# Performance work log

Measured on AMD Instinct MI355X. Metric: run time of the kernel, lower is better.

Reference implementation:

```python
import jax, jax.numpy as jnp
import numpy as np

N, NFEAT, NHID, NHEADS, NCLASS = 4096, 64, 64, 4, 64
ALPHA = 0.2        # LeakyReLU negative slope
NEG = -9.0e15      # mask value from the torch code (-9e15)


def _xavier(key, shape, gain=1.414):
    fan_in, fan_out = shape[-2] if len(shape) > 1 else shape[-1], shape[-1]
    if len(shape) == 1:
        fan_in, fan_out = shape[0], 1
    bound = gain * np.sqrt(6.0 / (fan_in + fan_out))
    return jax.random.uniform(key, shape, jnp.float32, -bound, bound)


def setup_inputs() -> dict:
    key = jax.random.key(0)
    ks = jax.random.split(key, 6)
    x = jax.random.normal(ks[0], (N, NFEAT), jnp.float32)
    # sparse-ish adjacency mask with self loops (adj > 0 gating in torch code)
    adj = jax.random.bernoulli(ks[1], 0.02, (N, N)) | jnp.eye(N, dtype=bool)
    W_heads = _xavier(ks[2], (NHEADS, NFEAT, NHID))                  # per-head W
    a_heads = _xavier(ks[3], (NHEADS, 2 * NHID))                     # per-head a (flattened [2F',1])
    W_out = _xavier(ks[4], (NHEADS * NHID, NCLASS))
    a_out = _xavier(ks[5], (2 * NCLASS,))
    return {"x": x, "W_heads": W_heads, "a_heads": a_heads,
            "W_out": W_out, "a_out": a_out, "adj": adj}


def gat_layer(x, adj, W, a, concat):
    # h: [N, F']
    h = x @ W
    Fp = h.shape[-1]
    # e_ij = leakyrelu(a[:F'].h_i + a[F':].h_j)  == torch's cat([h_i, h_j]) @ a
    f1 = h @ a[:Fp]                 # [N]
    f2 = h @ a[Fp:]                 # [N]
    e = jax.nn.leaky_relu(f1[:, None] + f2[None, :], ALPHA)   # [N, N]
    att = jax.nn.softmax(jnp.where(adj, e, NEG), axis=1)      # row softmax over neighbors
    hp = att @ h                    # [N, F']
    return jax.nn.elu(hp) if concat else hp


def reference(x, W_heads, a_heads, W_out, a_out, adj):
    # multi-head GAT with concat (dropout omitted: eval mode)
    heads = jax.vmap(lambda W, a: gat_layer(x, adj, W, a, True))(W_heads, a_heads)  # [H, N, F']
    hcat = jnp.transpose(heads, (1, 0, 2)).reshape(x.shape[0], NHEADS * NHID)       # [N, H*F']
    out = gat_layer(hcat, adj, W_out, a_out, False)                                  # [N, nclass]
    return out
```

## Files before the change

kernel.cpp:

```cpp
#include <hip/hip_runtime.h>
#include <hip/hip_fp16.h>

#define N 4096
#define CAP 160
#define ALPHA 0.2f
#define NSCAN 1024

__device__ __forceinline__ float wred_sum(float v) {
#pragma unroll
  for (int o = 32; o > 0; o >>= 1) v += __shfl_xor(v, o, 64);
  return v;
}

__device__ __forceinline__ void h8_fma(float4 raw, float p, float* acc) {
  union { float4 f4; __half2 h2[4]; } u;
  u.f4 = raw;
#pragma unroll
  for (int t = 0; t < 4; ++t) {
    float2 v = __half22float2(u.h2[t]);
    acc[2 * t]     = fmaf(p, v.x, acc[2 * t]);
    acc[2 * t + 1] = fmaf(p, v.y, acc[2 * t + 1]);
  }
}

__global__ void stage1_k(const void* __restrict__ adjv, const float* __restrict__ x,
                         const float* __restrict__ W, const float* __restrict__ a,
                         int* __restrict__ cnt, int* __restrict__ cols,
                         __half* __restrict__ h1, float* __restrict__ f1h,
                         float* __restrict__ f2h) {
  __shared__ float Ws[64 * 64];
  __shared__ float xs[4][64];
  int bid = blockIdx.x;
  int tid = threadIdx.x;
  int lane = tid & 63;
  if (bid < NSCAN) {
    int w = tid >> 6;
    int i = bid * 4 + w;
    int* mycols = cols + (size_t)i * CAP;
    const unsigned char* adjB = (const unsigned char*)adjv;
    bool byteLayout = (adjB[(size_t)N + 1] == 1);
    unsigned long long lt = (lane == 0) ? 0ull : (~0ull >> (64 - lane));
    int base = 0;
#define SCAN_ROUND(cond, jj)                                              \
    {                                                                     \
      unsigned long long m = __ballot(cond);                              \
      if (cond) {                                                         \
        int p = base + __popcll(m & lt);                                  \
        if (p < CAP) mycols[p] = (jj);                                    \
      }                                                                   \
      base += __popcll(m);                                                \
    }
    if (byteLayout) {
      const uint4* row4 = (const uint4*)(adjB + (size_t)i * N);
      uint4 v0 = row4[lane];
      uint4 v1 = row4[64 + lane];
      uint4 v2 = row4[128 + lane];
      uint4 v3 = row4[192 + lane];
#define SCAN_WORD(u, j0)                                                  \
      SCAN_ROUND(((u) & 0xffu) != 0, (j0));                               \
      SCAN_ROUND(((u) & 0xff00u) != 0, (j0) + 1);                         \
      SCAN_ROUND(((u) & 0xff0000u) != 0, (j0) + 2);                       \
      SCAN_ROUND(((u) & 0xff000000u) != 0, (j0) + 3);
#define SCAN_UINT4(v, it)                                                 \
      {                                                                   \
        int j0 = ((it) * 64 + lane) * 16;                                 \
        SCAN_WORD((v).x, j0);                                             \
        SCAN_WORD((v).y, j0 + 4);                                         \
        SCAN_WORD((v).z, j0 + 8);                                         \
        SCAN_WORD((v).w, j0 + 12);                                        \
      }
      SCAN_UINT4(v0, 0);
      SCAN_UINT4(v1, 1);
      SCAN_UINT4(v2, 2);
      SCAN_UINT4(v3, 3);
    } else {
      const int4* row = (const int4*)((const int*)adjv + (size_t)i * N);
      int4 nxt = row[lane];
      for (int it = 0; it < 16; ++it) {
        int4 cur = nxt;
        if (it < 15) nxt = row[(it + 1) * 64 + lane];
        int j0 = (it * 64 + lane) * 4;
        SCAN_ROUND(cur.x != 0, j0);
        SCAN_ROUND(cur.y != 0, j0 + 1);
        SCAN_ROUND(cur.z != 0, j0 + 2);
        SCAN_ROUND(cur.w != 0, j0 + 3);
      }
    }
    if (lane == 0) cnt[i] = min(base, CAP);
#undef SCAN_UINT4
#undef SCAN_WORD
#undef SCAN_ROUND
  } else {
    int u = bid - NSCAN;
    int h = u & 3;
    int r = tid >> 6, f = lane;
    int n = (u >> 2) * 4 + r;
    const float4* W4 = (const float4*)(W + h * 4096);
    float4* Ws4 = (float4*)Ws;
    for (int t = tid; t < 1024; t += 256) Ws4[t] = W4[t];
    xs[r][f] = x[(size_t)n * 64 + f];
    __syncthreads();
    float acc = 0.f;
#pragma unroll
    for (int k = 0; k < 64; k += 4) {
      float4 xk = *(const float4*)&xs[r][k];
      acc = fmaf(xk.x, Ws[k * 64 + f], acc);
      acc = fmaf(xk.y, Ws[(k + 1) * 64 + f], acc);
      acc = fmaf(xk.z, Ws[(k + 2) * 64 + f], acc);
      acc = fmaf(xk.w, Ws[(k + 3) * 64 + f], acc);
    }
    h1[((size_t)h * N + n) * 64 + f] = __float2half(acc);
    float s1 = wred_sum(acc * a[h * 128 + f]);
    float s2 = wred_sum(acc * a[h * 128 + 64 + f]);
    if (f == 0) { f1h[n * 4 + h] = s1; f2h[n * 4 + h] = s2; }
  }
}

__global__ void attn1_gemm_k(const int* __restrict__ cnt, const int* __restrict__ cols,
                             const __half* __restrict__ h1,
                             const float* __restrict__ f1g,
                             const float* __restrict__ f2g,
                             const float* __restrict__ Wout,
                             const float* __restrict__ aout,
                             __half* __restrict__ h2, float* __restrict__ f1o,
                             float* __restrict__ f2o) {
  int i0 = blockIdx.x * 2;
  int i1 = i0 + 1;
  int tid = threadIdx.x;
  int w = tid >> 6, lane = tid & 63;
  __shared__ int cS[2][CAP];
  __shared__ float pS[2][4][CAP];
  __shared__ float red[4][2][4];
  __shared__ float sDinv[2][4];
  __shared__ float hrow[2][256];
  __shared__ float4 part4[2][4][16];
  int c0 = cnt[i0], c1 = cnt[i1];
  float4 t10 = ((const float4*)f1g)[i0];
  float4 t11 = ((const float4*)f1g)[i1];
  float f1r[2][4] = {{t10.x, t10.y, t10.z, t10.w}, {t11.x, t11.y, t11.z, t11.w}};
  float dloc[2][4] = {{0.f, 0.f, 0.f, 0.f}, {0.f, 0.f, 0.f, 0.f}};
#pragma unroll
  for (int rr = 0; rr < 2; ++rr) {
    int c = rr ? c1 : c0;
    int ii = rr ? i1 : i0;
    for (int k = tid; k < c; k += 256) {
      int j = cols[(size_t)ii * CAP + k];
      cS[rr][k] = j;
      float4 t2 = ((const float4*)f2g)[j];
      float f2v[4] = {t2.x, t2.y, t2.z, t2.w};
#pragma unroll
      for (int h = 0; h < 4; ++h) {
        float s = f1r[rr][h] + f2v[h];
        s = s > 0.f ? s : ALPHA * s;
        float p = __expf(s);
        pS[rr][h][k] = p;
        dloc[rr][h] += p;
      }
    }
  }
#pragma unroll
  for (int rr = 0; rr < 2; ++rr)
#pragma unroll
    for (int h = 0; h < 4; ++h) {
      float d = wred_sum(dloc[rr][h]);
      if (lane == 0) red[w][rr][h] = d;
    }
  __syncthreads();
  if (tid < 8) {
    int rr = tid >> 2, h = tid & 3;
    float d = red[0][rr][h] + red[1][rr][h] + red[2][rr][h] + red[3][rr][h];
    int c = rr ? c1 : c0;
    sDinv[rr][h] = (c > 0) ? 1.f / d : 0.f;
  }
  __syncthreads();
  int g = lane >> 3, ff = lane & 7, h = w;
  const __half* hb = h1 + ((size_t)h * N) * 64;
  float a0[8] = {0.f, 0.f, 0.f, 0.f, 0.f, 0.f, 0.f, 0.f};
  float a1[8] = {0.f, 0.f, 0.f, 0.f, 0.f, 0.f, 0.f, 0.f};
  int cmax = c0 > c1 ? c0 : c1;
#pragma unroll 2
  for (int k0 = 0; k0 < cmax; k0 += 8) {
    int k = k0 + g;
    bool o0 = k < c0, o1 = k < c1;
    int j0 = o0 ? cS[0][k] : 0, j1 = o1 ? cS[1][k] : 0;
    float p0 = o0 ? pS[0][h][k] : 0.f, p1 = o1 ? pS[1][h][k] : 0.f;
    float4 r0 = *(const float4*)(hb + (size_t)j0 * 64 + ff * 8);
    float4 r1 = *(const float4*)(hb + (size_t)j1 * 64 + ff * 8);
    h8_fma(r0, p0, a0);
    h8_fma(r1, p1, a1);
  }
#pragma unroll
  for (int o = 8; o < 64; o <<= 1)
#pragma unroll
    for (int e = 0; e < 8; ++e) {
      a0[e] += __shfl_xor(a0[e], o, 64);
      a1[e] += __shfl_xor(a1[e], o, 64);
    }
  if (g == 0) {
    float d0 = sDinv[0][h], d1 = sDinv[1][h];
#pragma unroll
    for (int e = 0; e < 8; ++e) {
      float v0 = a0[e] * d0;
      float v1 = a1[e] * d1;
      v0 = v0 > 0.f ? v0 : expm1f(v0);
      v1 = v1 > 0.f ? v1 : expm1f(v1);
      hrow[0][h * 64 + ff * 8 + e] = v0;
      hrow[1][h * 64 + ff * 8 + e] = v1;
    }
  }
  __syncthreads();
  int ko = lane >> 4, f4 = lane & 15;
  float4 wa0 = {0.f, 0.f, 0.f, 0.f}, wa1 = wa0;
#pragma unroll
  for (int kk = 0; kk < 64; kk += 4) {
    int k = w * 64 + kk + ko;
    float4 wv = *(const float4*)(Wout + (size_t)k * 64 + f4 * 4);
    float h0 = hrow[0][k], h1v = hrow[1][k];
    wa0.x = fmaf(h0, wv.x, wa0.x); wa0.y = fmaf(h0, wv.y, wa0.y);
    wa0.z = fmaf(h0, wv.z, wa0.z); wa0.w = fmaf(h0, wv.w, wa0.w);
    wa1.x = fmaf(h1v, wv.x, wa1.x); wa1.y = fmaf(h1v, wv.y, wa1.y);
    wa1.z = fmaf(h1v, wv.z, wa1.z); wa1.w = fmaf(h1v, wv.w, wa1.w);
  }
#pragma unroll
  for (int o = 16; o < 64; o <<= 1) {
    wa0.x += __shfl_xor(wa0.x, o, 64); wa0.y += __shfl_xor(wa0.y, o, 64);
    wa0.z += __shfl_xor(wa0.z, o, 64); wa0.w += __shfl_xor(wa0.w, o, 64);
    wa1.x += __shfl_xor(wa1.x, o, 64); wa1.y += __shfl_xor(wa1.y, o, 64);
    wa1.z += __shfl_xor(wa1.z, o, 64); wa1.w += __shfl_xor(wa1.w, o, 64);
  }
  if (ko == 0) { part4[0][w][f4] = wa0; part4[1][w][f4] = wa1; }
  __syncthreads();
  if (tid < 32) {
    int rr = tid >> 4, fi = tid & 15;
    float4 s0 = part4[rr][0][fi], s1_ = part4[rr][1][fi];
    float4 s2_ = part4[rr][2][fi], s3_ = part4[rr][3][fi];
    float4 s = {(s0.x + s1_.x) + (s2_.x + s3_.x), (s0.y + s1_.y) + (s2_.y + s3_.y),
                (s0.z + s1_.z) + (s2_.z + s3_.z), (s0.w + s1_.w) + (s2_.w + s3_.w)};
    int i = rr ? i1 : i0;
    __half2* dst = (__half2*)(h2 + (size_t)i * 64 + fi * 4);
    dst[0] = __floats2half2_rn(s.x, s.y);
    dst[1] = __floats2half2_rn(s.z, s.w);
    float4 aA = *(const float4*)(aout + fi * 4);
    float4 aB = *(const float4*)(aout + 64 + fi * 4);
    float s1 = s.x * aA.x + s.y * aA.y + s.z * aA.z + s.w * aA.w;
    float s2 = s.x * aB.x + s.y * aB.y + s.z * aB.z + s.w * aB.w;
#pragma unroll
    for (int o = 1; o < 16; o <<= 1) {
      s1 += __shfl_xor(s1, o, 64);
      s2 += __shfl_xor(s2, o, 64);
    }
    if (fi == 0) { f1o[i] = s1; f2o[i] = s2; }
  }
}

__global__ void attn2_k(const int* __restrict__ cnt, const int* __restrict__ cols,
                        const __half* __restrict__ h2,
                        const float* __restrict__ f1g,
                        const float* __restrict__ f2g,
                        float* __restrict__ outf) {
  int tid = threadIdx.x;
  int w = tid >> 6, lane = tid & 63;
  int i = blockIdx.x * 4 + w;
  __shared__ int cS[4][CAP];
  __shared__ float pS[4][CAP];
  int c = cnt[i];
  float f1i = f1g[i];
  float dloc = 0.f;
  for (int k = lane; k < c; k += 64) {
    int j = cols[(size_t)i * CAP + k];
    cS[w][k] = j;
    float s = f1i + f2g[j];
    s = s > 0.f ? s : ALPHA * s;
    float p = __expf(s);
    pS[w][k] = p;
    dloc += p;
  }
  float dtot = wred_sum(dloc);
  float dinv = (c > 0) ? 1.f / dtot : 0.f;
  int g = lane >> 3, ff = lane & 7;
  float acc[8] = {0.f, 0.f, 0.f, 0.f, 0.f, 0.f, 0.f, 0.f};
#pragma unroll 2
  for (int k0 = 0; k0 < c; k0 += 8) {
    int k = k0 + g;
    bool o = k < c;
    int j = o ? cS[w][k] : 0;
    float p = o ? pS[w][k] : 0.f;
    float4 rv = *(const float4*)(h2 + (size_t)j * 64 + ff * 8);
    h8_fma(rv, p, acc);
  }
#pragma unroll
  for (int o = 8; o < 64; o <<= 1)
#pragma unroll
    for (int e = 0; e < 8; ++e) acc[e] += __shfl_xor(acc[e], o, 64);
  if (g == 0) {
    float4 v0 = {acc[0] * dinv, acc[1] * dinv, acc[2] * dinv, acc[3] * dinv};
    float4 v1 = {acc[4] * dinv, acc[5] * dinv, acc[6] * dinv, acc[7] * dinv};
    float* dst = outf + (size_t)i * 64 + ff * 8;
    *(float4*)dst = v0;
    *(float4*)(dst + 4) = v1;
  }
}

extern "C" void kernel_launch(void* const* d_in, const int* in_sizes, int n_in,
                              void* d_out, int out_size, void* d_ws, size_t ws_size,
                              hipStream_t stream) {
  const float* x    = (const float*)d_in[0];
  const float* Wh   = (const float*)d_in[1];
  const float* ah   = (const float*)d_in[2];
  const float* Wout = (const float*)d_in[3];
  const float* aout = (const float*)d_in[4];
  const void*  adj  = d_in[5];

  char* ws = (char*)d_ws;
  int* cnt  = (int*)ws;   ws += (size_t)N * sizeof(int);
  int* cols = (int*)ws;   ws += (size_t)N * CAP * sizeof(int);
  __half* h1 = (__half*)ws; ws += (size_t)N * 256 * sizeof(__half);
  float* f1h  = (float*)ws; ws += (size_t)N * 4 * sizeof(float);
  float* f2h  = (float*)ws; ws += (size_t)N * 4 * sizeof(float);
  __half* h2 = (__half*)ws; ws += (size_t)N * 64 * sizeof(__half);
  float* f1o  = (float*)ws; ws += (size_t)N * sizeof(float);
  float* f2o  = (float*)ws; ws += (size_t)N * sizeof(float);
  (void)in_sizes; (void)n_in; (void)out_size; (void)ws_size;

  stage1_k<<<NSCAN + 2 * N / 2, 256, 0, stream>>>(adj, x, Wh, ah, cnt, cols, h1,
                                                  f1h, f2h);
  attn1_gemm_k<<<N / 2, 256, 0, stream>>>(cnt, cols, h1, f1h, f2h, Wout, aout,
                                          h2, f1o, f2o);
  attn2_k<<<N / 4, 256, 0, stream>>>(cnt, cols, h2, f1o, f2o, (float*)d_out);
}
```

Before: 141.0 us.

## Fuse three GAT stages into one persistent cooperative kernel with grid syncs

Combines the adjacency scan/projection, first attention layer with output GEMM, and second attention layer into a single persistent cooperative kernel. Blocks loop over work units and two grid-wide barriers replace the kernel boundaries. This removes two launch gaps and the tail effects between stages. In exchange, shared memory for all three stages is allocated at once, which may limit occupancy, and grid syncs add their own overhead. The old three-kernel path is kept as a fallback.

After: 391.7 us. 178% more time.

```diff
diff --git a/kernel.cpp b/kernel.cpp
--- a/kernel.cpp
+++ b/kernel.cpp
@@ -1,4 +1,5 @@
 #include <hip/hip_runtime.h>
+#include <hip/hip_cooperative_groups.h>
 #include <hip/hip_fp16.h>
 
 #define N 4096
@@ -6,6 +7,8 @@
 #define ALPHA 0.2f
 #define NSCAN 1024
 
+namespace cg = cooperative_groups;
+
 __device__ __forceinline__ float wred_sum(float v) {
 #pragma unroll
   for (int o = 32; o > 0; o >>= 1) v += __shfl_xor(v, o, 64);
@@ -23,117 +26,115 @@
   }
 }
 
-__global__ void stage1_k(const void* __restrict__ adjv, const float* __restrict__ x,
-                         const float* __restrict__ W, const float* __restrict__ a,
-                         int* __restrict__ cnt, int* __restrict__ cols,
-                         __half* __restrict__ h1, float* __restrict__ f1h,
-                         float* __restrict__ f2h) {
-  __shared__ float Ws[64 * 64];
-  __shared__ float xs[4][64];
-  int bid = blockIdx.x;
-  int tid = threadIdx.x;
-  int lane = tid & 63;
-  if (bid < NSCAN) {
-    int w = tid >> 6;
-    int i = bid * 4 + w;
-    int* mycols = cols + (size_t)i * CAP;
-    const unsigned char* adjB = (const unsigned char*)adjv;
-    bool byteLayout = (adjB[(size_t)N + 1] == 1);
-    unsigned long long lt = (lane == 0) ? 0ull : (~0ull >> (64 - lane));
-    int base = 0;
+struct G1Smem { float Ws[64 * 64]; float xs[4][64]; };
+struct A1Smem {
+  int cS[2][CAP]; float pS[2][4][CAP]; float red[4][2][4];
+  float sDinv[2][4]; float hrow[2][256]; float4 part4[2][4][16];
+};
+struct A2Smem { int cS[4][CAP]; float pS[4][CAP]; };
+
+
+__device__ __forceinline__ void scan_unit(const void* __restrict__ adjv,
+                                          int* __restrict__ cnt,
+                                          int* __restrict__ cols,
+                                          int u, int tid) {
+  int w = tid >> 6, lane = tid & 63;
+  int i = u * 4 + w;
+  int* mycols = cols + (size_t)i * CAP;
+  const unsigned char* adjB = (const unsigned char*)adjv;
+  bool byteLayout = (adjB[(size_t)N + 1] == 1);
+  unsigned long long lt = (lane == 0) ? 0ull : (~0ull >> (64 - lane));
+  int base = 0;
 #define SCAN_ROUND(cond, jj)                                              \
+  {                                                                       \
+    unsigned long long m = __ballot(cond);                                \
+    if (cond) {                                                           \
+      int p = base + __popcll(m & lt);                                    \
+      if (p < CAP) mycols[p] = (jj);                                      \
+    }                                                                     \
+    base += __popcll(m);                                                  \
+  }
+  if (byteLayout) {
+    const uint4* row4 = (const uint4*)(adjB + (size_t)i * N);
+    uint4 v0 = row4[lane];
+    uint4 v1 = row4[64 + lane];
+    uint4 v2 = row4[128 + lane];
+    uint4 v3 = row4[192 + lane];
+#define SCAN_WORD(u_, j0)                                                 \
+    SCAN_ROUND(((u_) & 0xffu) != 0, (j0));                                \
+    SCAN_ROUND(((u_) & 0xff00u) != 0, (j0) + 1);                          \
+    SCAN_ROUND(((u_) & 0xff0000u) != 0, (j0) + 2);                        \
+    SCAN_ROUND(((u_) & 0xff000000u) != 0, (j0) + 3);
+#define SCAN_UINT4(v, it)                                                 \
     {                                                                     \
-      unsigned long long m = __ballot(cond);                              \
-      if (cond) {                                                         \
-        int p = base + __popcll(m & lt);                                  \
-        if (p < CAP) mycols[p] = (jj);                                    \
-      }                                                                   \
-      base += __popcll(m);                                                \
-    }
-    if (byteLayout) {
-      const uint4* row4 = (const uint4*)(adjB + (size_t)i * N);
-      uint4 v0 = row4[lane];
-      uint4 v1 = row4[64 + lane];
-      uint4 v2 = row4[128 + lane];
-      uint4 v3 = row4[192 + lane];
-#define SCAN_WORD(u, j0)                                                  \
-      SCAN_ROUND(((u) & 0xffu) != 0, (j0));                               \
-      SCAN_ROUND(((u) & 0xff00u) != 0, (j0) + 1);                         \
-      SCAN_ROUND(((u) & 0xff0000u) != 0, (j0) + 2);                       \
-      SCAN_ROUND(((u) & 0xff000000u) != 0, (j0) + 3);
-#define SCAN_UINT4(v, it)                                                 \
-      {                                                                   \
-        int j0 = ((it) * 64 + lane) * 16;                                 \
-        SCAN_WORD((v).x, j0);                                             \
-        SCAN_WORD((v).y, j0 + 4);                                         \
-        SCAN_WORD((v).z, j0 + 8);                                         \
-        SCAN_WORD((v).w, j0 + 12);                                        \
-      }
-      SCAN_UINT4(v0, 0);
-      SCAN_UINT4(v1, 1);
-      SCAN_UINT4(v2, 2);
-      SCAN_UINT4(v3, 3);
-    } else {
-      const int4* row = (const int4*)((const int*)adjv + (size_t)i * N);
-      int4 nxt = row[lane];
-      for (int it = 0; it < 16; ++it) {
-        int4 cur = nxt;
-        if (it < 15) nxt = row[(it + 1) * 64 + lane];
-        int j0 = (it * 64 + lane) * 4;
-        SCAN_ROUND(cur.x != 0, j0);
-        SCAN_ROUND(cur.y != 0, j0 + 1);
-        SCAN_ROUND(cur.z != 0, j0 + 2);
-        SCAN_ROUND(cur.w != 0, j0 + 3);
-      }
-    }
-    if (lane == 0) cnt[i] = min(base, CAP);
+      int j0 = ((it) * 64 + lane) * 16;                                   \
+      SCAN_WORD((v).x, j0);                                               \
+      SCAN_WORD((v).y, j0 + 4);                                           \
+      SCAN_WORD((v).z, j0 + 8);                                           \
+      SCAN_WORD((v).w, j0 + 12);                                          \
+    }
+    SCAN_UINT4(v0, 0);
+    SCAN_UINT4(v1, 1);
+    SCAN_UINT4(v2, 2);
+    SCAN_UINT4(v3, 3);
 #undef SCAN_UINT4
 #undef SCAN_WORD
+  } else {
+    const int4* row = (const int4*)((const int*)adjv + (size_t)i * N);
+    int4 nxt = row[lane];
+    for (int it = 0; it < 16; ++it) {
+      int4 cur = nxt;
+      if (it < 15) nxt = row[(it + 1) * 64 + lane];
+      int j0 = (it * 64 + lane) * 4;
+      SCAN_ROUND(cur.x != 0, j0);
+      SCAN_ROUND(cur.y != 0, j0 + 1);
+      SCAN_ROUND(cur.z != 0, j0 + 2);
+      SCAN_ROUND(cur.w != 0, j0 + 3);
+    }
+  }
 #undef SCAN_ROUND
-  } else {
-    int u = bid - NSCAN;
-    int h = u & 3;
-    int r = tid >> 6, f = lane;
-    int n = (u >> 2) * 4 + r;
-    const float4* W4 = (const float4*)(W + h * 4096);
-    float4* Ws4 = (float4*)Ws;
-    for (int t = tid; t < 1024; t += 256) Ws4[t] = W4[t];
-    xs[r][f] = x[(size_t)n * 64 + f];
-    __syncthreads();
-    float acc = 0.f;
-#pragma unroll
-    for (int k = 0; k < 64; k += 4) {
-      float4 xk = *(const float4*)&xs[r][k];
-      acc = fmaf(xk.x, Ws[k * 64 + f], acc);
-      acc = fmaf(xk.y, Ws[(k + 1) * 64 + f], acc);
-      acc = fmaf(xk.z, Ws[(k + 2) * 64 + f], acc);
-      acc = fmaf(xk.w, Ws[(k + 3) * 64 + f], acc);
-    }
-    h1[((size_t)h * N + n) * 64 + f] = __float2half(acc);
-    float s1 = wred_sum(acc * a[h * 128 + f]);
-    float s2 = wred_sum(acc * a[h * 128 + 64 + f]);
-    if (f == 0) { f1h[n * 4 + h] = s1; f2h[n * 4 + h] = s2; }
-  }
-}
-
-__global__ void attn1_gemm_k(const int* __restrict__ cnt, const int* __restrict__ cols,
-                             const __half* __restrict__ h1,
-                             const float* __restrict__ f1g,
-                             const float* __restrict__ f2g,
-                             const float* __restrict__ Wout,
-                             const float* __restrict__ aout,
-                             __half* __restrict__ h2, float* __restrict__ f1o,
-                             float* __restrict__ f2o) {
-  int i0 = blockIdx.x * 2;
+  if (lane == 0) cnt[i] = min(base, CAP);
+}
+
+__device__ __forceinline__ void gemm_unit(const float* __restrict__ x,
+                                          const float* __restrict__ W,
+                                          const float* __restrict__ a,
+                                          __half* __restrict__ h1,
+                                          float* __restrict__ f1h,
+                                          float* __restrict__ f2h,
+                                          int u, int tid, G1Smem& sm) {
+  int h = u & 3;
+  int r = tid >> 6, f = tid & 63;
+  int n = (u >> 2) * 4 + r;
+  const float4* W4 = (const float4*)(W + h * 4096);
+  float4* Ws4 = (float4*)sm.Ws;
+  for (int t = tid; t < 1024; t += 256) Ws4[t] = W4[t];
+  sm.xs[r][f] = x[(size_t)n * 64 + f];
+  __syncthreads();
+  float acc = 0.f;
+#pragma unroll
+  for (int k = 0; k < 64; k += 4) {
+    float4 xk = *(const float4*)&sm.xs[r][k];
+    acc = fmaf(xk.x, sm.Ws[k * 64 + f], acc);
+    acc = fmaf(xk.y, sm.Ws[(k + 1) * 64 + f], acc);
+    acc = fmaf(xk.z, sm.Ws[(k + 2) * 64 + f], acc);
+    acc = fmaf(xk.w, sm.Ws[(k + 3) * 64 + f], acc);
+  }
+  h1[((size_t)h * N + n) * 64 + f] = __float2half(acc);
+  float s1 = wred_sum(acc * a[h * 128 + f]);
+  float s2 = wred_sum(acc * a[h * 128 + 64 + f]);
+  if (f == 0) { f1h[n * 4 + h] = s1; f2h[n * 4 + h] = s2; }
+}
+
+__device__ __forceinline__ void attn1_unit(
+    const int* __restrict__ cnt, const int* __restrict__ cols,
+    const __half* __restrict__ h1, const float* __restrict__ f1g,
+    const float* __restrict__ f2g, const float* __restrict__ Wout,
+    const float* __restrict__ aout, __half* __restrict__ h2,
+    float* __restrict__ f1o, float* __restrict__ f2o, int i0, int tid,
+    A1Smem& sm) {
   int i1 = i0 + 1;
-  int tid = threadIdx.x;
   int w = tid >> 6, lane = tid & 63;
-  __shared__ int cS[2][CAP];
-  __shared__ float pS[2][4][CAP];
-  __shared__ float red[4][2][4];
-  __shared__ float sDinv[2][4];
-  __shared__ float hrow[2][256];
-  __shared__ float4 part4[2][4][16];
   int c0 = cnt[i0], c1 = cnt[i1];
   float4 t10 = ((const float4*)f1g)[i0];
   float4 t11 = ((const float4*)f1g)[i1];
@@ -145,7 +146,7 @@
     int ii = rr ? i1 : i0;
     for (int k = tid; k < c; k += 256) {
       int j = cols[(size_t)ii * CAP + k];
-      cS[rr][k] = j;
+      sm.cS[rr][k] = j;
       float4 t2 = ((const float4*)f2g)[j];
       float f2v[4] = {t2.x, t2.y, t2.z, t2.w};
 #pragma unroll
@@ -153,7 +154,7 @@
         float s = f1r[rr][h] + f2v[h];
         s = s > 0.f ? s : ALPHA * s;
         float p = __expf(s);
-        pS[rr][h][k] = p;
+        sm.pS[rr][h][k] = p;
         dloc[rr][h] += p;
       }
     }
@@ -163,14 +164,14 @@
 #pragma unroll
     for (int h = 0; h < 4; ++h) {
       float d = wred_sum(dloc[rr][h]);
-      if (lane == 0) red[w][rr][h] = d;
+      if (lane == 0) sm.red[w][rr][h] = d;
     }
   __syncthreads();
   if (tid < 8) {
     int rr = tid >> 2, h = tid & 3;
-    float d = red[0][rr][h] + red[1][rr][h] + red[2][rr][h] + red[3][rr][h];
+    float d = sm.red[0][rr][h] + sm.red[1][rr][h] + sm.red[2][rr][h] + sm.red[3][rr][h];
     int c = rr ? c1 : c0;
-    sDinv[rr][h] = (c > 0) ? 1.f / d : 0.f;
+    sm.sDinv[rr][h] = (c > 0) ? 1.f / d : 0.f;
   }
   __syncthreads();
   int g = lane >> 3, ff = lane & 7, h = w;
@@ -182,8 +183,8 @@
   for (int k0 = 0; k0 < cmax; k0 += 8) {
     int k = k0 + g;
     bool o0 = k < c0, o1 = k < c1;
-    int j0 = o0 ? cS[0][k] : 0, j1 = o1 ? cS[1][k] : 0;
-    float p0 = o0 ? pS[0][h][k] : 0.f, p1 = o1 ? pS[1][h][k] : 0.f;
+    int j0 = o0 ? sm.cS[0][k] : 0, j1 = o1 ? sm.cS[1][k] : 0;
+    float p0 = o0 ? sm.pS[0][h][k] : 0.f, p1 = o1 ? sm.pS[1][h][k] : 0.f;
     float4 r0 = *(const float4*)(hb + (size_t)j0 * 64 + ff * 8);
     float4 r1 = *(const float4*)(hb + (size_t)j1 * 64 + ff * 8);
     h8_fma(r0, p0, a0);
@@ -197,15 +198,15 @@
       a1[e] += __shfl_xor(a1[e], o, 64);
     }
   if (g == 0) {
-    float d0 = sDinv[0][h], d1 = sDinv[1][h];
+    float d0 = sm.sDinv[0][h], d1 = sm.sDinv[1][h];
 #pragma unroll
     for (int e = 0; e < 8; ++e) {
       float v0 = a0[e] * d0;
       float v1 = a1[e] * d1;
       v0 = v0 > 0.f ? v0 : expm1f(v0);
       v1 = v1 > 0.f ? v1 : expm1f(v1);
-      hrow[0][h * 64 + ff * 8 + e] = v0;
-      hrow[1][h * 64 + ff * 8 + e] = v1;
+      sm.hrow[0][h * 64 + ff * 8 + e] = v0;
+      sm.hrow[1][h * 64 + ff * 8 + e] = v1;
     }
   }
   __syncthreads();
@@ -215,7 +216,7 @@
   for (int kk = 0; kk < 64; kk += 4) {
     int k = w * 64 + kk + ko;
     float4 wv = *(const float4*)(Wout + (size_t)k * 64 + f4 * 4);
-    float h0 = hrow[0][k], h1v = hrow[1][k];
+    float h0 = sm.hrow[0][k], h1v = sm.hrow[1][k];
     wa0.x = fmaf(h0, wv.x, wa0.x); wa0.y = fmaf(h0, wv.y, wa0.y);
     wa0.z = fmaf(h0, wv.z, wa0.z); wa0.w = fmaf(h0, wv.w, wa0.w);
     wa1.x = fmaf(h1v, wv.x, wa1.x); wa1.y = fmaf(h1v, wv.y, wa1.y);
@@ -228,12 +229,12 @@
     wa1.x += __shfl_xor(wa1.x, o, 64); wa1.y += __shfl_xor(wa1.y, o, 64);
     wa1.z += __shfl_xor(wa1.z, o, 64); wa1.w += __shfl_xor(wa1.w, o, 64);
   }
-  if (ko == 0) { part4[0][w][f4] = wa0; part4[1][w][f4] = wa1; }
+  if (ko == 0) { sm.part4[0][w][f4] = wa0; sm.part4[1][w][f4] = wa1; }
   __syncthreads();
   if (tid < 32) {
     int rr = tid >> 4, fi = tid & 15;
-    float4 s0 = part4[rr][0][fi], s1_ = part4[rr][1][fi];
-    float4 s2_ = part4[rr][2][fi], s3_ = part4[rr][3][fi];
+    float4 s0 = sm.part4[rr][0][fi], s1_ = sm.part4[rr][1][fi];
+    float4 s2_ = sm.part4[rr][2][fi], s3_ = sm.part4[rr][3][fi];
     float4 s = {(s0.x + s1_.x) + (s2_.x + s3_.x), (s0.y + s1_.y) + (s2_.y + s3_.y),
                 (s0.z + s1_.z) + (s2_.z + s3_.z), (s0.w + s1_.w) + (s2_.w + s3_.w)};
     int i = rr ? i1 : i0;
@@ -253,26 +254,23 @@
   }
 }
 
-__global__ void attn2_k(const int* __restrict__ cnt, const int* __restrict__ cols,
-                        const __half* __restrict__ h2,
-                        const float* __restrict__ f1g,
-                        const float* __restrict__ f2g,
-                        float* __restrict__ outf) {
-  int tid = threadIdx.x;
+__device__ __forceinline__ void attn2_unit(
+    const int* __restrict__ cnt, const int* __restrict__ cols,
+    const __half* __restrict__ h2, const float* __restrict__ f1g,
+    const float* __restrict__ f2g, float* __restrict__ outf, int u, int tid,
+    A2Smem& sm) {
   int w = tid >> 6, lane = tid & 63;
-  int i = blockIdx.x * 4 + w;
-  __shared__ int cS[4][CAP];
-  __shared__ float pS[4][CAP];
+  int i = u * 4 + w;
   int c = cnt[i];
   float f1i = f1g[i];
   float dloc = 0.f;
   for (int k = lane; k < c; k += 64) {
     int j = cols[(size_t)i * CAP + k];
-    cS[w][k] = j;
+    sm.cS[w][k] = j;
     float s = f1i + f2g[j];
     s = s > 0.f ? s : ALPHA * s;
     float p = __expf(s);
-    pS[w][k] = p;
+    sm.pS[w][k] = p;
     dloc += p;
   }
   float dtot = wred_sum(dloc);
@@ -283,8 +281,8 @@
   for (int k0 = 0; k0 < c; k0 += 8) {
     int k = k0 + g;
     bool o = k < c;
-    int j = o ? cS[w][k] : 0;
-    float p = o ? pS[w][k] : 0.f;
+    int j = o ? sm.cS[w][k] : 0;
+    float p = o ? sm.pS[w][k] : 0.f;
     float4 rv = *(const float4*)(h2 + (size_t)j * 64 + ff * 8);
     h8_fma(rv, p, acc);
   }
@@ -301,15 +299,74 @@
   }
 }
 
+__global__ __launch_bounds__(256, 4) void fused_k(
+    const void* __restrict__ adjv, const float* __restrict__ x,
+    const float* __restrict__ W, const float* __restrict__ a,
+    const float* __restrict__ Wout, const float* __restrict__ aout,
+    int* __restrict__ cnt, int* __restrict__ cols, __half* __restrict__ h1,
+    float* __restrict__ f1h, float* __restrict__ f2h, __half* __restrict__ h2,
+    float* __restrict__ f1o, float* __restrict__ f2o, float* __restrict__ outf,
+    int nblk) {
+  __shared__ G1Smem g1;
+  __shared__ A1Smem sa1;
+  __shared__ A2Smem sa2;
+  int tid = threadIdx.x;
+  cg::grid_group grid = cg::this_grid();
+  for (int u = blockIdx.x; u < NSCAN + N; u += nblk) {
+    if (u < NSCAN) scan_unit(adjv, cnt, cols, u, tid);
+    else gemm_unit(x, W, a, h1, f1h, f2h, u - NSCAN, tid, g1);
+    __syncthreads();
+  }
+  __threadfence();
+  grid.sync();
+  for (int p = blockIdx.x; p < N / 2; p += nblk) {
+    attn1_unit(cnt, cols, h1, f1h, f2h, Wout, aout, h2, f1o, f2o, p * 2, tid, sa1);
+    __syncthreads();
+  }
+  __threadfence();
+  grid.sync();
+  for (int q = blockIdx.x; q < N / 4; q += nblk) {
+    attn2_unit(cnt, cols, h2, f1o, f2o, outf, q, tid, sa2);
+  }
+}
+
+__global__ void stage1_k(const void* __restrict__ adjv, const float* __restrict__ x,
+                         const float* __restrict__ W, const float* __restrict__ a,
+                         int* __restrict__ cnt, int* __restrict__ cols,
+                         __half* __restrict__ h1, float* __restrict__ f1h,
+                         float* __restrict__ f2h) {
+  __shared__ G1Smem g1;
+  int bid = blockIdx.x, tid = threadIdx.x;
+  if (bid < NSCAN) scan_unit(adjv, cnt, cols, bid, tid);
+  else gemm_unit(x, W, a, h1, f1h, f2h, bid - NSCAN, tid, g1);
+}
+
+__global__ void attn1_gemm_k(const int* __restrict__ cnt, const int* __restrict__ cols,
+                             const __half* __restrict__ h1, const float* __restrict__ f1g,
+                             const float* __restrict__ f2g, const float* __restrict__ Wout,
+                             const float* __restrict__ aout, __half* __restrict__ h2,
+                             float* __restrict__ f1o, float* __restrict__ f2o) {
+  __shared__ A1Smem sm;
+  attn1_unit(cnt, cols, h1, f1g, f2g, Wout, aout, h2, f1o, f2o, blockIdx.x * 2,
+             threadIdx.x, sm);
+}
+
+__global__ void attn2_k(const int* __restrict__ cnt, const int* __restrict__ cols,
+                        const __half* __restrict__ h2, const float* __restrict__ f1g,
+                        const float* __restrict__ f2g, float* __restrict__ outf) {
+  __shared__ A2Smem sm;
+  attn2_unit(cnt, cols, h2, f1g, f2g, outf, blockIdx.x, threadIdx.x, sm);
+}
+
 extern "C" void kernel_launch(void* const* d_in, const int* in_sizes, int n_in,
                               void* d_out, int out_size, void* d_ws, size_t ws_size,
                               hipStream_t stream) {
+  const void*  adj  = d_in[5];
   const float* x    = (const float*)d_in[0];
   const float* Wh   = (const float*)d_in[1];
   const float* ah   = (const float*)d_in[2];
   const float* Wout = (const float*)d_in[3];
   const float* aout = (const float*)d_in[4];
-  const void*  adj  = d_in[5];
 
   char* ws = (char*)d_ws;
   int* cnt  = (int*)ws;   ws += (size_t)N * sizeof(int);
@@ -320,11 +377,30 @@
   __half* h2 = (__half*)ws; ws += (size_t)N * 64 * sizeof(__half);
   float* f1o  = (float*)ws; ws += (size_t)N * sizeof(float);
   float* f2o  = (float*)ws; ws += (size_t)N * sizeof(float);
+  float* outf = (float*)d_out;
   (void)in_sizes; (void)n_in; (void)out_size; (void)ws_size;
 
-  stage1_k<<<NSCAN + 2 * N / 2, 256, 0, stream>>>(adj, x, Wh, ah, cnt, cols, h1,
-                                                  f1h, f2h);
+  static int nblk_s = 0;
+  if (nblk_s == 0) {
+    int occ = 0;
+    hipError_t oe = hipOccupancyMaxActiveBlocksPerMultiprocessor(
+        &occ, (const void*)fused_k, 256, 0);
+    if (oe != hipSuccess || occ < 1) nblk_s = -1;
+    else nblk_s = (occ * 256 > 1024) ? 1024 : occ * 256;
+  }
+  if (nblk_s > 0) {
+    int nblk = nblk_s;
+    void* args[] = {(void*)&adj, (void*)&x, (void*)&Wh, (void*)&ah,
+                    (void*)&Wout, (void*)&aout, (void*)&cnt, (void*)&cols,
+                    (void*)&h1, (void*)&f1h, (void*)&f2h, (void*)&h2,
+                    (void*)&f1o, (void*)&f2o, (void*)&outf, (void*)&nblk};
+    hipError_t e = hipLaunchCooperativeKernel((const void*)fused_k, dim3(nblk),
+                                              dim3(256), args, 0, stream);
+    if (e == hipSuccess) return;
+    nblk_s = -1;
+  }
+  stage1_k<<<NSCAN + N, 256, 0, stream>>>(adj, x, Wh, ah, cnt, cols, h1, f1h, f2h);
   attn1_gemm_k<<<N / 2, 256, 0, stream>>>(cnt, cols, h1, f1h, f2h, Wout, aout,
                                           h2, f1o, f2o);
-  attn2_k<<<N / 4, 256, 0, stream>>>(cnt, cols, h2, f1o, f2o, (float*)d_out);
-}
+  attn2_k<<<N / 4, 256, 0, stream>>>(cnt, cols, h2, f1o, f2o, outf);
+}
```
